# Kernel tuning notes

Measured on AMD Instinct MI355X. Metric: run time of the kernel, lower is better.

## Reference

```python
import jax, jax.numpy as jnp
import numpy as np

# Module constants (from init_kwargs / source defaults)
SIG_BASELINE = 100.0
R1 = 1.0
R1CA = 4.3
FA = 10.0
TR = 0.00487
STEP = 0.1          # fine time-grid step used inside _param_to_conc_tcm_SnB
DELAY = int(3 / STEP)  # 30-sample bolus delay
H = W = 320


def setup_inputs() -> dict:
    key = jax.random.key(0)
    k1, k2 = jax.random.split(key)
    # ve, vp, fp, ps maps; positive so Te/T/Tc and the discriminant are well-defined
    param = jax.random.uniform(k1, (4, H, W), jnp.float32, minval=0.05, maxval=1.0)
    sample_time = jnp.arange(50, dtype=jnp.float32) * 1.2  # 50 frames, t_end = 58.8
    Cp = jax.random.uniform(k2, (50,), jnp.float32)        # arterial input fn samples
    return {"param": param, "sample_time": sample_time, "Cp": Cp}


def _nan0(x):
    return jnp.where(jnp.isnan(x), jnp.zeros_like(x), x)


def _conc_tcm(param, t_samp, aif):
    # param: [4,H,W]; t_samp: [L]; aif: [L] (delayed, interpolated AIF)
    ve, vp, fp, ps = param[0], param[1], param[2], param[3]
    Te = _nan0(ve / ps)
    T = _nan0((vp + ve) / fp)
    Tc = _nan0(vp / fp)
    disc = jnp.sqrt((T + Te) ** 2 - 4.0 * Tc * Te)
    theta_p = _nan0((T + Te + disc) / (2.0 * Tc * Te))
    theta_m = _nan0((T + Te - disc) / (2.0 * Tc * Te))

    t_map = t_samp[:, None, None]                       # [L,1,1]
    em = jnp.exp(-t_map * theta_m)                      # [L,H,W]
    ep = jnp.exp(-t_map * theta_p)
    denom = theta_p - theta_m
    pref = theta_p * theta_m
    he = pref * (em - ep) / denom
    hp = pref * ((1.0 - Te * theta_m) * em + (Te * theta_p - 1.0) * ep) / denom
    he = _nan0(he / jnp.sum(he, axis=0, keepdims=True))
    hp = _nan0(hp / jnp.sum(hp, axis=0, keepdims=True))

    # Batched full FFT convolution along time (replaces per-pixel scipy loop).
    L = t_samp.shape[0]
    Lfull = 2 * L - 1
    aif_f = jnp.fft.rfft(aif, n=Lfull)                  # [F]
    ce = jnp.fft.irfft(aif_f[:, None, None] * jnp.fft.rfft(he, n=Lfull, axis=0),
                       n=Lfull, axis=0)[:L]             # conv 'full', truncated to [:L]
    cp = jnp.fft.irfft(aif_f[:, None, None] * jnp.fft.rfft(hp, n=Lfull, axis=0),
                       n=Lfull, axis=0)[:L]
    return vp * cp + ve * ce                            # [L,H,W]


def reference(param, sample_time, Cp):
    # Fine time grid (static length; sample_time built with known spacing)
    t_end = float(np.asarray(sample_time)[-1])
    L = int(round(t_end / STEP)) + 1
    t_samp = jnp.arange(L, dtype=jnp.float32) * STEP

    # pchip_interpolate -> linear interp (see notes); then 3s bolus delay
    aifci = jnp.interp(t_samp, sample_time, Cp)
    aif = jnp.concatenate([jnp.zeros((DELAY,), aifci.dtype), aifci[:-DELAY]])

    conc = _conc_tcm(param, t_samp, aif)                # [L,H,W]

    # Select fine-grid samples closest-after each measurement time
    idx = jnp.searchsorted(t_samp, sample_time, side='left')  # [T]
    CA = conc[idx][:, None, :, :]                       # [T,1,H,W]

    # Signal model (SPGR)
    fa = FA * np.pi / 180.0
    cosf, sinf = jnp.cos(jnp.float32(fa)), jnp.sin(jnp.float32(fa))
    E1 = jnp.exp(jnp.float32(-TR * R1))
    M0 = SIG_BASELINE * (1.0 - cosf * E1) / (sinf * (1.0 - E1))
    M0_trans = M0 * sinf
    M_steady = M0_trans * (1.0 - E1) / (1.0 - E1 * cosf)

    E1CA = jnp.exp(-TR * (R1 + R1CA * CA))
    CA_trans = M0_trans * (1.0 - E1CA) / (1.0 - E1CA * cosf)
    sig = CA_trans + (SIG_BASELINE - M_steady)
    return sig                                          # [T,1,H,W]
```

## Files before the change

### kernel.cpp

```cpp
#include <hip/hip_runtime.h>
#include <math.h>

#define L_TOT   589
#define L_PAD   592
#define NCHUNK  (L_PAD / 8)
#define NDELAY  30
#define NSAMP   50
#define HW_PIX  102400
#define STEPF   0.1f
#define BLK     64

__global__ __launch_bounds__(BLK) void dce_kernel(
    const float* __restrict__ param,
    const float* __restrict__ st_g,
    const float* __restrict__ cp_g,
    float* __restrict__ out,
    float M0_trans, float cos_fa, float sig_base)
{
    __shared__ __align__(16) float s_aif[L_PAD];
    __shared__ float s_st[NSAMP], s_cp[NSAMP];
    __shared__ int   s_idx[NSAMP];

    const int tid = threadIdx.x;
    if (tid < NSAMP) { s_st[tid] = st_g[tid]; s_cp[tid] = cp_g[tid]; }
    __syncthreads();

    for (int k = tid; k < L_PAD; k += BLK) {
        float v = 0.0f;
        if (k >= NDELAY && k < L_TOT) {
            float t = (float)(k - NDELAY) * STEPF;
            int j = (k - NDELAY) / 12;
            if (j > NSAMP - 2) j = NSAMP - 2;
            if (s_st[j + 1] <= t) ++j;
            if (j > 0 && s_st[j] > t) --j;
            v = s_cp[j] + (t - s_st[j]) * (s_cp[j + 1] - s_cp[j])
                        / (s_st[j + 1] - s_st[j]);
        }
        s_aif[k] = v;
    }
    if (tid < NSAMP) {
        float sv = s_st[tid];
        int lo = 12 * tid - 2; if (lo < 0) lo = 0;
        int cnt = lo;
        for (int n = lo; n <= 12 * tid + 2; ++n)
            if ((float)n * STEPF < sv) cnt = n + 1;
        s_idx[tid] = min(cnt, L_TOT - 1);
    }
    __syncthreads();

    const int pix = blockIdx.x * BLK + tid;
    const float ve = param[0 * HW_PIX + pix];
    const float vp = param[1 * HW_PIX + pix];
    const float fp = param[2 * HW_PIX + pix];
    const float ps = param[3 * HW_PIX + pix];

    const float Te = ve / ps;
    const float T  = (vp + ve) / fp;
    const float Tc = vp / fp;
    const float sm = T + Te;
    const float disc = sqrtf(sm * sm - 4.0f * Tc * Te);
    const float den2 = 2.0f * Tc * Te;
    const float thp = (sm + disc) / den2;
    const float thm = (sm - disc) / den2;

    const float rm = expf(-STEPF * thm);
    const float rp = expf(-STEPF * thp);

    const float Se = (1.0f - expf(-(STEPF * (float)L_TOT) * thm)) / (1.0f - rm);
    const float Sp = (1.0f - expf(-(STEPF * (float)L_TOT) * thp)) / (1.0f - rp);

    const float we  = 1.0f - Te * thm;
    const float wpp = Te * thp - 1.0f;
    const float inv_De = 1.0f / (Se - Sp);
    const float inv_Dp = 1.0f / (we * Se + wpp * Sp);

    float Sm = 0.0f, Spv = 0.0f;
    int s = 0;
    int next = __builtin_amdgcn_readfirstlane(s_idx[0]);

    const float4* aif4 = (const float4*)s_aif;
    float4 ca = aif4[0], cb = aif4[1];

    #pragma unroll 1
    for (int q = 0; q < NCHUNK; ++q) {
        float4 na = ca, nb = cb;
        if (q + 1 < NCHUNK) { na = aif4[2 * q + 2]; nb = aif4[2 * q + 3]; }
        const int base = q * 8;

#define DCE_STEP(A, U)                                                        \
        { const float a_ = (A);                                               \
          Sm  = fmaf(Sm,  rm, a_);                                            \
          Spv = fmaf(Spv, rp, a_);                                            \
          if (base + (U) == next) {               \
              const float ce_   = (Sm - Spv) * inv_De;                        \
              const float cpv_  = (we * Sm + wpp * Spv) * inv_Dp;             \
              const float conc_ = vp * cpv_ + ve * ce_;                       \
              const float E1CA_ = __expf(-0.00487f * fmaf(4.3f, conc_, 1.0f));\
              const float catr_ = M0_trans * (1.0f - E1CA_)                   \
                                / (1.0f - E1CA_ * cos_fa);                    \
              out[s * HW_PIX + pix] = catr_ + sig_base;                       \
              ++s;                                                            \
              next = (s < NSAMP) ? __builtin_amdgcn_readfirstlane(s_idx[s])   \
                                 : -1;                                        \
          } }

        DCE_STEP(ca.x, 0) DCE_STEP(ca.y, 1) DCE_STEP(ca.z, 2) DCE_STEP(ca.w, 3)
        DCE_STEP(cb.x, 4) DCE_STEP(cb.y, 5) DCE_STEP(cb.z, 6) DCE_STEP(cb.w, 7)
#undef DCE_STEP
        ca = na; cb = nb;
    }
}

extern "C" void kernel_launch(void* const* d_in, const int* in_sizes, int n_in,
                              void* d_out, int out_size, void* d_ws, size_t ws_size,
                              hipStream_t stream) {
    const float* param = (const float*)d_in[0];
    const float* st    = (const float*)d_in[1];
    const float* Cp    = (const float*)d_in[2];
    float* out = (float*)d_out;

    double fa   = 10.0 * M_PI / 180.0;
    double cfa  = cos(fa), sfa = sin(fa);
    double E1   = exp(-0.00487);
    double M0   = 100.0 * (1.0 - cfa * E1) / (sfa * (1.0 - E1));
    double M0t  = M0 * sfa;
    double Mst  = M0t * (1.0 - E1) / (1.0 - E1 * cfa);
    float M0_trans = (float)M0t;
    float cos_fa   = (float)cfa;
    float sig_base = (float)(100.0 - Mst);

    dce_kernel<<<HW_PIX / BLK, BLK, 0, stream>>>(param, st, Cp, out,
                                                 M0_trans, cos_fa, sig_base);
}
```

Before: 85.96 us.

## Hoist AIF interpolation into a prep kernel and use fast reciprocals

The AIF interpolation and sample-index computation move out of every block into a separate single-block prep kernel that writes them to workspace. The main kernel then reads them from global memory (cached, wave-uniform) with a two-chunk prefetch instead of rebuilding them in LDS. Divisions and expf calls are also replaced by hardware reciprocal and fast exp intrinsics. The change removes per-block setup work and a barrier, but adds a second kernel launch, global loads in the inner loop, and lower-precision arithmetic.

```diff
diff --git a/kernel.cpp b/kernel.cpp
--- a/kernel.cpp
+++ b/kernel.cpp
@@ -10,22 +10,19 @@
 #define STEPF   0.1f
 #define BLK     64
 
-__global__ __launch_bounds__(BLK) void dce_kernel(
-    const float* __restrict__ param,
-    const float* __restrict__ st_g,
-    const float* __restrict__ cp_g,
-    float* __restrict__ out,
-    float M0_trans, float cos_fa, float sig_base)
+__device__ __forceinline__ float frcp(float x) { return __builtin_amdgcn_rcpf(x); }
+
+__global__ void prep_kernel(const float* __restrict__ st,
+                            const float* __restrict__ Cp,
+                            float* __restrict__ aif,
+                            int* __restrict__ idx)
 {
-    __shared__ __align__(16) float s_aif[L_PAD];
     __shared__ float s_st[NSAMP], s_cp[NSAMP];
-    __shared__ int   s_idx[NSAMP];
-
-    const int tid = threadIdx.x;
-    if (tid < NSAMP) { s_st[tid] = st_g[tid]; s_cp[tid] = cp_g[tid]; }
+    const int k = threadIdx.x;
+    if (k < NSAMP) { s_st[k] = st[k]; s_cp[k] = Cp[k]; }
     __syncthreads();
 
-    for (int k = tid; k < L_PAD; k += BLK) {
+    if (k < L_PAD) {
         float v = 0.0f;
         if (k >= NDELAY && k < L_TOT) {
             float t = (float)(k - NDELAY) * STEPF;
@@ -36,78 +33,89 @@
             v = s_cp[j] + (t - s_st[j]) * (s_cp[j + 1] - s_cp[j])
                         / (s_st[j + 1] - s_st[j]);
         }
-        s_aif[k] = v;
+        aif[k] = v;
     }
-    if (tid < NSAMP) {
-        float sv = s_st[tid];
-        int lo = 12 * tid - 2; if (lo < 0) lo = 0;
+    if (k < NSAMP) {
+        float sv = s_st[k];
+        int lo = 12 * k - 2; if (lo < 0) lo = 0;
         int cnt = lo;
-        for (int n = lo; n <= 12 * tid + 2; ++n)
+        for (int n = lo; n <= 12 * k + 2; ++n)
             if ((float)n * STEPF < sv) cnt = n + 1;
-        s_idx[tid] = min(cnt, L_TOT - 1);
+        idx[k] = min(cnt, L_TOT - 1);
     }
-    __syncthreads();
+}
 
-    const int pix = blockIdx.x * BLK + tid;
+__global__ __launch_bounds__(BLK) void dce_kernel(
+    const float* __restrict__ param,
+    const float* __restrict__ aif_g,
+    const int*   __restrict__ idx_g,
+    float* __restrict__ out,
+    float M0_trans, float cos_fa, float sig_base)
+{
+    const int pix = blockIdx.x * BLK + threadIdx.x;
     const float ve = param[0 * HW_PIX + pix];
     const float vp = param[1 * HW_PIX + pix];
     const float fp = param[2 * HW_PIX + pix];
     const float ps = param[3 * HW_PIX + pix];
 
-    const float Te = ve / ps;
-    const float T  = (vp + ve) / fp;
-    const float Tc = vp / fp;
-    const float sm = T + Te;
+    const float Te   = ve * frcp(ps);
+    const float rfp  = frcp(fp);
+    const float T    = (vp + ve) * rfp;
+    const float Tc   = vp * rfp;
+    const float sm   = T + Te;
     const float disc = sqrtf(sm * sm - 4.0f * Tc * Te);
-    const float den2 = 2.0f * Tc * Te;
-    const float thp = (sm + disc) / den2;
-    const float thm = (sm - disc) / den2;
+    const float rd2  = frcp(2.0f * Tc * Te);
+    const float thp  = (sm + disc) * rd2;
+    const float thm  = (sm - disc) * rd2;
 
-    const float rm = expf(-STEPF * thm);
-    const float rp = expf(-STEPF * thp);
+    const float rm = __expf(-STEPF * thm);
+    const float rp = __expf(-STEPF * thp);
 
-    const float Se = (1.0f - expf(-(STEPF * (float)L_TOT) * thm)) / (1.0f - rm);
-    const float Sp = (1.0f - expf(-(STEPF * (float)L_TOT) * thp)) / (1.0f - rp);
+    const float Se = (1.0f - __expf(-(STEPF * (float)L_TOT) * thm)) * frcp(1.0f - rm);
+    const float Sp = (1.0f - __expf(-(STEPF * (float)L_TOT) * thp)) * frcp(1.0f - rp);
 
     const float we  = 1.0f - Te * thm;
     const float wpp = Te * thp - 1.0f;
-    const float inv_De = 1.0f / (Se - Sp);
-    const float inv_Dp = 1.0f / (we * Se + wpp * Sp);
+    const float inv_De = frcp(Se - Sp);
+    const float inv_Dp = frcp(we * Se + wpp * Sp);
 
     float Sm = 0.0f, Spv = 0.0f;
     int s = 0;
-    int next = __builtin_amdgcn_readfirstlane(s_idx[0]);
+    int next  = __builtin_amdgcn_readfirstlane(idx_g[0]);
+    int next2 = __builtin_amdgcn_readfirstlane(idx_g[1]);
 
-    const float4* aif4 = (const float4*)s_aif;
-    float4 ca = aif4[0], cb = aif4[1];
+    const float4* aif4 = (const float4*)aif_g;
+    float4 c0 = aif4[0], c1 = aif4[1];
+    float4 n0 = aif4[2], n1 = aif4[3];
 
     #pragma unroll 1
     for (int q = 0; q < NCHUNK; ++q) {
-        float4 na = ca, nb = cb;
-        if (q + 1 < NCHUNK) { na = aif4[2 * q + 2]; nb = aif4[2 * q + 3]; }
+        float4 p0 = c0, p1 = c1;
+        if (q + 2 < NCHUNK) { p0 = aif4[2 * q + 4]; p1 = aif4[2 * q + 5]; }
         const int base = q * 8;
 
 #define DCE_STEP(A, U)                                                        \
         { const float a_ = (A);                                               \
           Sm  = fmaf(Sm,  rm, a_);                                            \
           Spv = fmaf(Spv, rp, a_);                                            \
-          if (base + (U) == next) {               \
+          if (base + (U) == next) {           \
               const float ce_   = (Sm - Spv) * inv_De;                        \
               const float cpv_  = (we * Sm + wpp * Spv) * inv_Dp;             \
               const float conc_ = vp * cpv_ + ve * ce_;                       \
-              const float E1CA_ = __expf(-0.00487f * fmaf(4.3f, conc_, 1.0f));\
-              const float catr_ = M0_trans * (1.0f - E1CA_)                   \
-                                / (1.0f - E1CA_ * cos_fa);                    \
+              const float E_    = __expf(-0.00487f * fmaf(4.3f, conc_, 1.0f));\
+              const float catr_ = M0_trans * (1.0f - E_)                      \
+                                * frcp(1.0f - E_ * cos_fa);                   \
               out[s * HW_PIX + pix] = catr_ + sig_base;                       \
               ++s;                                                            \
-              next = (s < NSAMP) ? __builtin_amdgcn_readfirstlane(s_idx[s])   \
-                                 : -1;                                        \
+              next = next2;                                                   \
+              next2 = (s + 1 < NSAMP)                                         \
+                    ? __builtin_amdgcn_readfirstlane(idx_g[s + 1]) : -1;      \
           } }
 
-        DCE_STEP(ca.x, 0) DCE_STEP(ca.y, 1) DCE_STEP(ca.z, 2) DCE_STEP(ca.w, 3)
-        DCE_STEP(cb.x, 4) DCE_STEP(cb.y, 5) DCE_STEP(cb.z, 6) DCE_STEP(cb.w, 7)
+        DCE_STEP(c0.x, 0) DCE_STEP(c0.y, 1) DCE_STEP(c0.z, 2) DCE_STEP(c0.w, 3)
+        DCE_STEP(c1.x, 4) DCE_STEP(c1.y, 5) DCE_STEP(c1.z, 6) DCE_STEP(c1.w, 7)
 #undef DCE_STEP
-        ca = na; cb = nb;
+        c0 = n0; c1 = n1; n0 = p0; n1 = p1;
     }
 }
 
@@ -119,6 +127,9 @@
     const float* Cp    = (const float*)d_in[2];
     float* out = (float*)d_out;
 
+    float* aif = (float*)d_ws;
+    int*   idx = (int*)((char*)d_ws + 4096);
+
     double fa   = 10.0 * M_PI / 180.0;
     double cfa  = cos(fa), sfa = sin(fa);
     double E1   = exp(-0.00487);
@@ -129,6 +140,7 @@
     float cos_fa   = (float)cfa;
     float sig_base = (float)(100.0 - Mst);
 
-    dce_kernel<<<HW_PIX / BLK, BLK, 0, stream>>>(param, st, Cp, out,
+    prep_kernel<<<1, L_PAD, 0, stream>>>(st, Cp, aif, idx);
+    dce_kernel<<<HW_PIX / BLK, BLK, 0, stream>>>(param, aif, idx, out,
                                                  M0_trans, cos_fa, sig_base);
 }
```

Result: slower. 92.60 us (+7.7%).
